# Optimization experiments

Hardware: AMD Instinct MI355X
Metric: run time of the kernel (lower is better)

Reference implementation:

```python
import jax, jax.numpy as jnp
import numpy as np

B, S, D = 4, 2048, 1024
O = 1024
E = 8
K = 2

def setup_inputs() -> dict:
    key = jax.random.key(0)
    k1, k2, k3, k4, k5 = jax.random.split(key, 5)
    scale = 1.0 / np.sqrt(D)
    x = jax.random.normal(k1, (B, S, D), dtype=jnp.float32)
    # expert linear layers stacked: weight [E, D, O], bias [E, O]
    We = jax.random.uniform(k2, (E, D, O), dtype=jnp.float32, minval=-scale, maxval=scale)
    be = jax.random.uniform(k3, (E, O), dtype=jnp.float32, minval=-scale, maxval=scale)
    # gate linear: weight [D, E], bias [E]
    Wg = jax.random.uniform(k4, (D, E), dtype=jnp.float32, minval=-scale, maxval=scale)
    bg = jax.random.uniform(k5, (E,), dtype=jnp.float32, minval=-scale, maxval=scale)
    return {"x": x, "We": We, "be": be, "Wg": Wg, "bg": bg}

def reference(x, We, be, Wg, bg):
    b, s, d = x.shape
    x_flat = x.reshape(-1, d)                                   # [N, D]
    gates = jax.nn.softmax(x_flat @ Wg + bg, axis=-1)           # [N, E]
    topk_gates, topk_idx = jax.lax.top_k(gates, K)              # [N, K]
    topk_gates = topk_gates / jnp.sum(topk_gates, axis=1, keepdims=True)
    # dense all-expert compute (faithful to original naive MoE)
    expert_out = jnp.einsum('nd,edo->neo', x_flat, We) + be     # [N, E, O]
    # gather top-k expert outputs per token
    selected = jnp.take_along_axis(expert_out, topk_idx[:, :, None], axis=1)  # [N, K, O]
    out = jnp.sum(selected * topk_gates[:, :, None], axis=1)    # [N, O]
    return out.reshape(b, s, -1)
```

## Files before the change

kernel.cpp:

```cpp
#include <hip/hip_runtime.h>

#define N_TOK 8192
#define DDIM 1024
#define ODIM 1024
#define NEXP 8

typedef __attribute__((ext_vector_type(8))) short bf16x8;
typedef __attribute__((ext_vector_type(4))) float f32x4;

__device__ __forceinline__ unsigned int f2bf(float f) {
    unsigned int u = __float_as_uint(f);
    return (u + 0x7fffu + ((u >> 16) & 1u)) >> 16;
}
__device__ __forceinline__ float bflo(unsigned int u) { return __uint_as_float(u << 16); }
__device__ __forceinline__ float bfhi(unsigned int u) { return __uint_as_float(u & 0xffff0000u); }

__device__ __forceinline__ void async_copy16(const unsigned short* g, unsigned short* l) {
    __builtin_amdgcn_global_load_lds(
        (const __attribute__((address_space(1))) unsigned int*)g,
        (__attribute__((address_space(3))) unsigned int*)l, 16, 0, 0);
}

__global__ __launch_bounds__(256) void prep_kernel(const float* __restrict__ x,
                                                   const float* __restrict__ Wg,
                                                   const float* __restrict__ bg,
                                                   const float* __restrict__ We,
                                                   int* __restrict__ ea, int* __restrict__ eb,
                                                   float* __restrict__ ga, float* __restrict__ gb,
                                                   unsigned short* __restrict__ xbf,
                                                   unsigned short* __restrict__ WeT,
                                                   int* __restrict__ counts) {
    __shared__ float tile[64][65];
    if (blockIdx.x < 2048) {
        if (blockIdx.x == 0) counts[threadIdx.x] = 0;
        const int wave = threadIdx.x >> 6, lane = threadIdx.x & 63;
        const int t = blockIdx.x * 4 + wave;
        const float* xr = x + (size_t)t * DDIM;

        float4 v[4];
#pragma unroll
        for (int c = 0; c < 4; ++c) v[c] = *(const float4*)&xr[c * 256 + lane * 4];

        unsigned short* xo = xbf + (size_t)t * DDIM;
#pragma unroll
        for (int c = 0; c < 4; ++c) {
            uint2 w;
            w.x = f2bf(v[c].x) | (f2bf(v[c].y) << 16);
            w.y = f2bf(v[c].z) | (f2bf(v[c].w) << 16);
            *(uint2*)&xo[c * 256 + lane * 4] = w;
        }

        float acc[8] = {0, 0, 0, 0, 0, 0, 0, 0};
#pragma unroll
        for (int c = 0; c < 4; ++c) {
            const int dbase = c * 256 + lane * 4;
#pragma unroll
            for (int j = 0; j < 4; ++j) {
                float xv = ((const float*)&v[c])[j];
                const float4* w = (const float4*)(Wg + (size_t)(dbase + j) * 8);
                float4 w0 = w[0], w1 = w[1];
                acc[0] += xv * w0.x; acc[1] += xv * w0.y; acc[2] += xv * w0.z; acc[3] += xv * w0.w;
                acc[4] += xv * w1.x; acc[5] += xv * w1.y; acc[6] += xv * w1.z; acc[7] += xv * w1.w;
            }
        }
#pragma unroll
        for (int off = 32; off > 0; off >>= 1) {
#pragma unroll
            for (int j = 0; j < 8; ++j) acc[j] += __shfl_xor(acc[j], off, 64);
        }
        if (lane == 0) {
            float s[8];
#pragma unroll
            for (int e = 0; e < 8; ++e) s[e] = acc[e] + bg[e];
            int a = 0;
#pragma unroll
            for (int e = 1; e < 8; ++e) if (s[e] > s[a]) a = e;
            int b = (a == 0) ? 1 : 0;
#pragma unroll
            for (int e = 0; e < 8; ++e) if (e != a && e != b && s[e] > s[b]) b = e;
            float g0 = 1.0f / (1.0f + __expf(s[b] - s[a]));
            ea[t] = a; eb[t] = b; ga[t] = g0; gb[t] = 1.0f - g0;
        }
    } else {
        const int lin = blockIdx.x - 2048;
        const int e = lin >> 8, rem = lin & 255;
        const int d0 = (rem >> 4) * 64, o0 = (rem & 15) * 64;
        const int tid = threadIdx.x;
#pragma unroll
        for (int p = 0; p < 4; ++p) {
            int idx = p * 256 + tid;
            int row = idx >> 4, c = idx & 15;
            float4 v = *(const float4*)&We[(((size_t)e * 1024 + d0 + row) << 10) + o0 + (c << 2)];
            tile[row][c * 4 + 0] = v.x; tile[row][c * 4 + 1] = v.y;
            tile[row][c * 4 + 2] = v.z; tile[row][c * 4 + 3] = v.w;
        }
        __syncthreads();
#pragma unroll
        for (int p = 0; p < 2; ++p) {
            int idx = p * 256 + tid;
            int orow = idx >> 3, c8 = idx & 7;
            unsigned int u[8];
#pragma unroll
            for (int j = 0; j < 8; ++j) u[j] = f2bf(tile[c8 * 8 + j][orow]);
            uint4 q;
            q.x = u[0] | (u[1] << 16); q.y = u[2] | (u[3] << 16);
            q.z = u[4] | (u[5] << 16); q.w = u[6] | (u[7] << 16);
            *(uint4*)&WeT[(((size_t)e * 1024 + o0 + orow) << 10) + d0 + (c8 << 3)] = q;
        }
    }
}

__global__ __launch_bounds__(64) void scatter_kernel(const int* __restrict__ ea,
                                                     const int* __restrict__ eb,
                                                     int* __restrict__ counts,
                                                     int* __restrict__ btok,
                                                     int* __restrict__ slotA,
                                                     int* __restrict__ slotB) {
    const int t = blockIdx.x * 64 + threadIdx.x;
    const int lane = threadIdx.x & 63;
#pragma unroll
    for (int pass = 0; pass < 2; ++pass) {
        const int e = (pass == 0) ? ea[t] : eb[t];
        int* slot = (pass == 0) ? slotA : slotB;
#pragma unroll
        for (int ex = 0; ex < NEXP; ++ex) {
            unsigned long long mask = __ballot(e == ex);
            if (mask) {
                int leader = __ffsll((long long)mask) - 1;
                int base = 0;
                if (lane == leader) base = atomicAdd(&counts[ex * 32], __popcll(mask));
                base = __shfl(base, leader, 64);
                if (e == ex) {
                    int pos = base + __popcll(mask & ((1ull << lane) - 1ull));
                    btok[ex * N_TOK + pos] = t;
                    slot[t] = ex * N_TOK + pos;
                }
            }
        }
    }
}

__global__ __launch_bounds__(512, 2) void moe_gemm(const unsigned short* __restrict__ xbf,
                                                   const unsigned short* __restrict__ WeT,
                                                   const float* __restrict__ be,
                                                   const int* __restrict__ counts,
                                                   const int* __restrict__ btok,
                                                   unsigned short* __restrict__ ybuf) {
    const int id = blockIdx.x;
    const int e = id & 7;
    const int n0 = ((id >> 3) & 3) * 256;
    const int r0 = (id >> 5) * 256;
    const int cnt = counts[e * 32];
    if (r0 >= cnt) return;

    __shared__ unsigned short sA[2][256 * 64];
    __shared__ unsigned short sB[2][256 * 64];
    __shared__ int s_tok[256];

    const int tid = threadIdx.x;
    if (tid < 256) {
        int r = r0 + tid;
        int rc = (r < cnt) ? r : (cnt - 1);
        s_tok[tid] = btok[e * N_TOK + rc];
    }
    const int w = tid >> 6, lane = tid & 63;
    __syncthreads();

    const int rsub = lane >> 3;
    const int colo = ((lane & 7) ^ rsub) * 8;
    unsigned int a_off[4], b_off[4];
#pragma unroll
    for (int p = 0; p < 4; ++p) {
        int row = p * 64 + w * 8 + rsub;
        a_off[p] = ((unsigned)s_tok[row] << 10) + colo;
        b_off[p] = ((unsigned)(e * 1024 + n0 + row) << 10) + colo;
    }

    const int wm = (w >> 2) * 128, wn = (w & 3) * 64;
    const int quad = lane >> 4, rA = lane & 15;
    const int sw = rA & 7;

    f32x4 acc[8][4];
#pragma unroll
    for (int mi = 0; mi < 8; ++mi)
#pragma unroll
        for (int ni = 0; ni < 4; ++ni) acc[mi][ni] = (f32x4){0.f, 0.f, 0.f, 0.f};

#pragma unroll
    for (int p = 0; p < 4; ++p) {
        async_copy16(xbf + a_off[p], &sA[0][(p * 64 + w * 8) * 64]);
        async_copy16(WeT + b_off[p], &sB[0][(p * 64 + w * 8) * 64]);
    }
    __syncthreads();

    int buf = 0;
    for (int kb = 0; kb < 16; ++kb) {
        if (kb < 15) {
            const int ko = (kb + 1) * 64;
            const int nb = buf ^ 1;
#pragma unroll
            for (int p = 0; p < 4; ++p) {
                async_copy16(xbf + a_off[p] + ko, &sA[nb][(p * 64 + w * 8) * 64]);
                async_copy16(WeT + b_off[p] + ko, &sB[nb][(p * 64 + w * 8) * 64]);
            }
        }
#pragma unroll
        for (int ks = 0; ks < 2; ++ks) {
            const int cslot = ((ks * 4 + quad) ^ sw) * 8;
            bf16x8 bfr[4];
#pragma unroll
            for (int ni = 0; ni < 4; ++ni)
                bfr[ni] = *(bf16x8*)&sB[buf][(wn + ni * 16 + rA) * 64 + cslot];
#pragma unroll
            for (int mi = 0; mi < 8; ++mi) {
                bf16x8 af = *(bf16x8*)&sA[buf][(wm + mi * 16 + rA) * 64 + cslot];
#pragma unroll
                for (int ni = 0; ni < 4; ++ni)
                    acc[mi][ni] = __builtin_amdgcn_mfma_f32_16x16x32_bf16(af, bfr[ni], acc[mi][ni], 0, 0, 0);
            }
        }
        __syncthreads();
        buf ^= 1;
    }

#pragma unroll
    for (int ni = 0; ni < 4; ++ni) {
        int col = n0 + wn + ni * 16 + rA;
        float bias = be[(e << 10) + col];
#pragma unroll
        for (int mi = 0; mi < 8; ++mi) {
#pragma unroll
            for (int r = 0; r < 4; ++r) {
                int lrow = wm + mi * 16 + quad * 4 + r;
                if (r0 + lrow < cnt) {
                    ybuf[(((size_t)(e * N_TOK + r0 + lrow)) << 10) + col] =
                        (unsigned short)f2bf(acc[mi][ni][r] + bias);
                }
            }
        }
    }
}

__global__ __launch_bounds__(256) void combine_kernel(const unsigned short* __restrict__ ybuf,
                                                      const int* __restrict__ slotA,
                                                      const int* __restrict__ slotB,
                                                      const float* __restrict__ ga,
                                                      const float* __restrict__ gb,
                                                      float* __restrict__ out) {
    const int wave = threadIdx.x >> 6, lane = threadIdx.x & 63;
    const int t = blockIdx.x * 4 + wave;
    const unsigned short* ra = ybuf + ((size_t)slotA[t] << 10);
    const unsigned short* rb = ybuf + ((size_t)slotB[t] << 10);
    const float a = ga[t], b = gb[t];
    float* orow = out + ((size_t)t << 10);
#pragma unroll
    for (int i = 0; i < 2; ++i) {
        int c = i * 512 + lane * 8;
        uint4 ua = *(const uint4*)&ra[c];
        uint4 ub = *(const uint4*)&rb[c];
        float4 o0, o1;
        o0.x = a * bflo(ua.x) + b * bflo(ub.x);
        o0.y = a * bfhi(ua.x) + b * bfhi(ub.x);
        o0.z = a * bflo(ua.y) + b * bflo(ub.y);
        o0.w = a * bfhi(ua.y) + b * bfhi(ub.y);
        o1.x = a * bflo(ua.z) + b * bflo(ub.z);
        o1.y = a * bfhi(ua.z) + b * bfhi(ub.z);
        o1.z = a * bflo(ua.w) + b * bflo(ub.w);
        o1.w = a * bfhi(ua.w) + b * bfhi(ub.w);
        *(float4*)&orow[c] = o0;
        *(float4*)&orow[c + 4] = o1;
    }
}

extern "C" void kernel_launch(void* const* d_in, const int* in_sizes, int n_in,
                              void* d_out, int out_size, void* d_ws, size_t ws_size,
                              hipStream_t stream) {
    const float* x  = (const float*)d_in[0];
    const float* We = (const float*)d_in[1];
    const float* be = (const float*)d_in[2];
    const float* Wg = (const float*)d_in[3];
    const float* bg = (const float*)d_in[4];
    float* out = (float*)d_out;

    char* ws = (char*)d_ws;
    size_t off = 0;
    int* counts = (int*)(ws + off); off += 8 * 32 * 4;
    int* btok   = (int*)(ws + off); off += NEXP * N_TOK * 4;
    int* slotA  = (int*)(ws + off); off += N_TOK * 4;
    int* slotB  = (int*)(ws + off); off += N_TOK * 4;
    int* ea = (int*)(ws + off); off += N_TOK * 4;
    int* eb = (int*)(ws + off); off += N_TOK * 4;
    float* ga = (float*)(ws + off); off += N_TOK * 4;
    float* gb = (float*)(ws + off); off += N_TOK * 4;
    unsigned short* WeT  = (unsigned short*)(ws + off); off += (size_t)NEXP * DDIM * ODIM * 2;
    unsigned short* xbf  = (unsigned short*)(ws + off); off += (size_t)N_TOK * DDIM * 2;
    unsigned short* ybuf = (unsigned short*)(ws + off); off += (size_t)NEXP * N_TOK * ODIM * 2;

    prep_kernel<<<dim3(4096), 256, 0, stream>>>(x, Wg, bg, We, ea, eb, ga, gb, xbf, WeT, counts);
    scatter_kernel<<<dim3(N_TOK / 64), 64, 0, stream>>>(ea, eb, counts, btok, slotA, slotB);
    moe_gemm<<<dim3(32 * 4 * 8), 512, 0, stream>>>(xbf, WeT, be, counts, btok, ybuf);
    combine_kernel<<<dim3(N_TOK / 4), 256, 0, stream>>>(ybuf, slotA, slotB, ga, gb, out);
}
```

Measured before the change: 247.3 us.

## Restructure MoE GEMM main loop with explicit waitcnt pipelining and vectorized epilogue

Rewrites the expert GEMM K-loop to issue the next tile's async global-to-LDS loads after the second half's fragments are read. It uses explicit vmcnt/lgkmcnt waits, raw s_barrier with sched_barrier fences and setprio around the MFMA bursts, so loads overlap compute with finer control than __syncthreads. The MFMA operand order is swapped so each lane holds four consecutive output columns, which lets the epilogue write packed bf16x4 stores with vectorized bias loads instead of scalar 2-byte stores. The hand-placed waits and barriers add correctness risk if the counts are off.

Result: faster. 222.1 us (-10.2%).

```diff
diff --git a/kernel.cpp b/kernel.cpp
--- a/kernel.cpp
+++ b/kernel.cpp
@@ -153,8 +153,7 @@
     const int cnt = counts[e * 32];
     if (r0 >= cnt) return;
 
-    __shared__ unsigned short sA[2][256 * 64];
-    __shared__ unsigned short sB[2][256 * 64];
+    __shared__ unsigned short smem[65536];
     __shared__ int s_tok[256];
 
     const int tid = threadIdx.x;
@@ -175,10 +174,13 @@
         a_off[p] = ((unsigned)s_tok[row] << 10) + colo;
         b_off[p] = ((unsigned)(e * 1024 + n0 + row) << 10) + colo;
     }
+    const int ldsrow = w * 8;
 
     const int wm = (w >> 2) * 128, wn = (w & 3) * 64;
     const int quad = lane >> 4, rA = lane & 15;
     const int sw = rA & 7;
+    const int cs0 = (quad ^ sw) * 8;
+    const int cs1 = ((4 + quad) ^ sw) * 8;
 
     f32x4 acc[8][4];
 #pragma unroll
@@ -188,54 +190,90 @@
 
 #pragma unroll
     for (int p = 0; p < 4; ++p) {
-        async_copy16(xbf + a_off[p], &sA[0][(p * 64 + w * 8) * 64]);
-        async_copy16(WeT + b_off[p], &sB[0][(p * 64 + w * 8) * 64]);
-    }
-    __syncthreads();
-
-    int buf = 0;
-    for (int kb = 0; kb < 16; ++kb) {
-        if (kb < 15) {
-            const int ko = (kb + 1) * 64;
-            const int nb = buf ^ 1;
+        async_copy16(xbf + a_off[p], &smem[(p * 64 + ldsrow) * 64]);
+        async_copy16(WeT + b_off[p], &smem[32768 + (p * 64 + ldsrow) * 64]);
+    }
+#pragma unroll
+    for (int p = 0; p < 4; ++p) {
+        async_copy16(xbf + a_off[p] + 64, &smem[16384 + (p * 64 + ldsrow) * 64]);
+        async_copy16(WeT + b_off[p] + 64, &smem[49152 + (p * 64 + ldsrow) * 64]);
+    }
+    asm volatile("s_waitcnt vmcnt(8)" ::: "memory");
+    __builtin_amdgcn_s_barrier();
+    __builtin_amdgcn_sched_barrier(0);
+
+    for (int t = 0; t < 16; ++t) {
+        const int cur = t & 1;
+        unsigned short* sAc = smem + cur * 16384;
+        unsigned short* sBc = smem + 32768 + cur * 16384;
+
+        bf16x8 a0[8], b0[4];
+#pragma unroll
+        for (int mi = 0; mi < 8; ++mi) a0[mi] = *(bf16x8*)&sAc[(wm + mi * 16 + rA) * 64 + cs0];
+#pragma unroll
+        for (int ni = 0; ni < 4; ++ni) b0[ni] = *(bf16x8*)&sBc[(wn + ni * 16 + rA) * 64 + cs0];
+        asm volatile("s_waitcnt lgkmcnt(0)" ::: "memory");
+        __builtin_amdgcn_sched_barrier(0);
+
+        __builtin_amdgcn_s_setprio(1);
+#pragma unroll
+        for (int mi = 0; mi < 8; ++mi)
+#pragma unroll
+            for (int ni = 0; ni < 4; ++ni)
+                acc[mi][ni] = __builtin_amdgcn_mfma_f32_16x16x32_bf16(b0[ni], a0[mi], acc[mi][ni], 0, 0, 0);
+        __builtin_amdgcn_s_setprio(0);
+
+        bf16x8 a1[8], b1[4];
+#pragma unroll
+        for (int mi = 0; mi < 8; ++mi) a1[mi] = *(bf16x8*)&sAc[(wm + mi * 16 + rA) * 64 + cs1];
+#pragma unroll
+        for (int ni = 0; ni < 4; ++ni) b1[ni] = *(bf16x8*)&sBc[(wn + ni * 16 + rA) * 64 + cs1];
+        asm volatile("s_waitcnt lgkmcnt(0)" ::: "memory");
+        __builtin_amdgcn_sched_barrier(0);
+        __builtin_amdgcn_s_barrier();
+        __builtin_amdgcn_sched_barrier(0);
+
+        if (t < 14) {
+            const int ko = (t + 2) * 64;
 #pragma unroll
             for (int p = 0; p < 4; ++p) {
-                async_copy16(xbf + a_off[p] + ko, &sA[nb][(p * 64 + w * 8) * 64]);
-                async_copy16(WeT + b_off[p] + ko, &sB[nb][(p * 64 + w * 8) * 64]);
+                async_copy16(xbf + a_off[p] + ko, &sAc[(p * 64 + ldsrow) * 64]);
+                async_copy16(WeT + b_off[p] + ko, &sBc[(p * 64 + ldsrow) * 64]);
             }
         }
-#pragma unroll
-        for (int ks = 0; ks < 2; ++ks) {
-            const int cslot = ((ks * 4 + quad) ^ sw) * 8;
-            bf16x8 bfr[4];
+
+        __builtin_amdgcn_s_setprio(1);
+#pragma unroll
+        for (int mi = 0; mi < 8; ++mi)
 #pragma unroll
             for (int ni = 0; ni < 4; ++ni)
-                bfr[ni] = *(bf16x8*)&sB[buf][(wn + ni * 16 + rA) * 64 + cslot];
-#pragma unroll
-            for (int mi = 0; mi < 8; ++mi) {
-                bf16x8 af = *(bf16x8*)&sA[buf][(wm + mi * 16 + rA) * 64 + cslot];
-#pragma unroll
-                for (int ni = 0; ni < 4; ++ni)
-                    acc[mi][ni] = __builtin_amdgcn_mfma_f32_16x16x32_bf16(af, bfr[ni], acc[mi][ni], 0, 0, 0);
-            }
-        }
-        __syncthreads();
-        buf ^= 1;
-    }
-
-#pragma unroll
-    for (int ni = 0; ni < 4; ++ni) {
-        int col = n0 + wn + ni * 16 + rA;
-        float bias = be[(e << 10) + col];
-#pragma unroll
-        for (int mi = 0; mi < 8; ++mi) {
-#pragma unroll
-            for (int r = 0; r < 4; ++r) {
-                int lrow = wm + mi * 16 + quad * 4 + r;
-                if (r0 + lrow < cnt) {
-                    ybuf[(((size_t)(e * N_TOK + r0 + lrow)) << 10) + col] =
-                        (unsigned short)f2bf(acc[mi][ni][r] + bias);
-                }
+                acc[mi][ni] = __builtin_amdgcn_mfma_f32_16x16x32_bf16(b1[ni], a1[mi], acc[mi][ni], 0, 0, 0);
+        __builtin_amdgcn_s_setprio(0);
+
+        if (t < 14) {
+            asm volatile("s_waitcnt vmcnt(8)" ::: "memory");
+            __builtin_amdgcn_s_barrier();
+            __builtin_amdgcn_sched_barrier(0);
+        } else if (t == 14) {
+            asm volatile("s_waitcnt vmcnt(0)" ::: "memory");
+            __builtin_amdgcn_s_barrier();
+            __builtin_amdgcn_sched_barrier(0);
+        }
+    }
+
+#pragma unroll
+    for (int mi = 0; mi < 8; ++mi) {
+        const int lrow = wm + mi * 16 + rA;
+        if (r0 + lrow < cnt) {
+            unsigned short* yrow =
+                ybuf + (((size_t)(e * N_TOK + r0 + lrow)) << 10) + n0 + wn + quad * 4;
+#pragma unroll
+            for (int ni = 0; ni < 4; ++ni) {
+                float4 bv = *(const float4*)&be[(e << 10) + n0 + wn + ni * 16 + quad * 4];
+                uint2 pk;
+                pk.x = f2bf(acc[mi][ni][0] + bv.x) | (f2bf(acc[mi][ni][1] + bv.y) << 16);
+                pk.y = f2bf(acc[mi][ni][2] + bv.z) | (f2bf(acc[mi][ni][3] + bv.w) << 16);
+                *(uint2*)&yrow[ni * 16] = pk;
             }
         }
     }
```
